# Kernel optimization log

Hardware: AMD Instinct MI355X
Metric: run time of the kernel (lower is better)

Reference implementation:

```python
import jax, jax.numpy as jnp
import numpy as np

C_IN = 256
C_INTER = C_IN // 2  # max(1, C//2)
B, D, H, W = 2, 16, 64, 64


def setup_inputs() -> dict:
    key = jax.random.key(0)
    ks = jax.random.split(key, 9)
    s = 1.0 / np.sqrt(C_IN)
    si = 1.0 / np.sqrt(C_INTER)
    return {
        "x": jax.random.normal(ks[0], (B, C_IN, D, H, W), dtype=jnp.float32),
        # 1x1x1 conv weights reduce to [out, in] matrices
        "g_w": jax.random.normal(ks[1], (C_INTER, C_IN), dtype=jnp.float32) * s,
        "g_b": jax.random.normal(ks[2], (C_INTER,), dtype=jnp.float32) * s,
        "theta_w": jax.random.normal(ks[3], (C_INTER, C_IN), dtype=jnp.float32) * s,
        "theta_b": jax.random.normal(ks[4], (C_INTER,), dtype=jnp.float32) * s,
        "phi_w": jax.random.normal(ks[5], (C_INTER, C_IN), dtype=jnp.float32) * s,
        "phi_b": jax.random.normal(ks[6], (C_INTER,), dtype=jnp.float32) * s,
        # note: torch code inits W to zero; random here so gradients/outputs are non-trivial
        "W_w": jax.random.normal(ks[7], (C_IN, C_INTER), dtype=jnp.float32) * si,
        "W_b": jax.random.normal(ks[8], (C_IN,), dtype=jnp.float32) * si,
    }


def reference(x, g_w, g_b, theta_w, theta_b, phi_w, phi_b, W_w, W_b):
    b, c, d, h, w = x.shape
    n = d * h * w
    xf = x.reshape(b, c, n)  # [B, C, N]
    # 1x1x1 convs == per-position linear projections
    g = jnp.einsum('oc,bcn->bon', g_w, xf) + g_b[None, :, None]        # [B, Ci, N]
    th = jnp.einsum('oc,bcn->bon', theta_w, xf) + theta_b[None, :, None]
    ph = jnp.einsum('oc,bcn->bon', phi_w, xf) + phi_b[None, :, None]
    # f = theta^T @ phi (N x N), y = (f / N) @ g^T. Since the normalizer is a
    # constant, reassociate: kv = phi @ g^T is [Ci, Ci], avoiding the NxN matrix.
    kv = jnp.einsum('bin,bjn->bij', ph, g)                              # [B, Ci, Ci]
    y = jnp.einsum('bin,bij->bjn', th, kv) / n                          # [B, Ci, N]
    y = jnp.einsum('oc,bcn->bon', W_w, y) + W_b[None, :, None]          # [B, C, N]
    return x + y.reshape(b, c, d, h, w)
```

## Files before the change

### kernel.cpp

```cpp
#include <hip/hip_runtime.h>

#define NB 2
#define CC 256
#define CI 128
#define NN 65536
#define LDA 72
#define LDX 264

typedef __bf16 bf16x8 __attribute__((ext_vector_type(8)));
typedef float f32x4 __attribute__((ext_vector_type(4)));

__device__ __forceinline__ unsigned short f2bf(float f) {
  unsigned u = __float_as_uint(f);
  u += 0x7fffu + ((u >> 16) & 1u);
  return (unsigned short)(u >> 16);
}

__global__ __launch_bounds__(512) void nl3d_syrk2(const float* __restrict__ x,
                                                  float* __restrict__ S,
                                                  float* __restrict__ partials,
                                                  float* __restrict__ svec,
                                                  int kchunk, int use_partial) {
  __shared__ unsigned short lds[256 * LDA];
  const int tid = threadIdx.x;
  const int lane = tid & 63;
  const int wv = tid >> 6;
  const int wm = wv & 3, wn = wv >> 2;
  const int b = blockIdx.y;
  const int kc0 = blockIdx.x * kchunk;

  const float* xb = x + (size_t)b * CC * NN;
  f32x4 acc[4][8];
  const f32x4 zero4 = {0.f, 0.f, 0.f, 0.f};
#pragma unroll
  for (int i = 0; i < 4; ++i)
#pragma unroll
    for (int j = 0; j < 8; ++j) acc[i][j] = zero4;

  float rsum[8];
#pragma unroll
  for (int i = 0; i < 8; ++i) rsum[i] = 0.f;

  const int r0 = tid >> 4;
  const int c4 = tid & 15;

  const int stages = kchunk >> 6;
  for (int s = 0; s < stages; ++s) {
    const int kc = kc0 + s * 64;
    float4 f[8];
#pragma unroll
    for (int i = 0; i < 8; ++i) {
      int row = r0 + 32 * i;
      f[i] = *(const float4*)(xb + (size_t)row * NN + kc + c4 * 4);
    }
    __syncthreads();
#pragma unroll
    for (int i = 0; i < 8; ++i) {
      int row = r0 + 32 * i;
      ushort4 h;
      h.x = f2bf(f[i].x); h.y = f2bf(f[i].y); h.z = f2bf(f[i].z); h.w = f2bf(f[i].w);
      *(ushort4*)&lds[row * LDA + c4 * 4] = h;
      rsum[i] += f[i].x + f[i].y + f[i].z + f[i].w;
    }
    __syncthreads();

    const int m = lane & 15;
    const int kg = (lane >> 4) * 8;
#pragma unroll
    for (int kk = 0; kk < 2; ++kk) {
      bf16x8 afr[4], bfr[8];
#pragma unroll
      for (int mt = 0; mt < 4; ++mt)
        afr[mt] = *(const bf16x8*)&lds[(wm * 64 + mt * 16 + m) * LDA + kk * 32 + kg];
#pragma unroll
      for (int nt = 0; nt < 8; ++nt)
        bfr[nt] = *(const bf16x8*)&lds[(wn * 128 + nt * 16 + m) * LDA + kk * 32 + kg];
#pragma unroll
      for (int mt = 0; mt < 4; ++mt)
#pragma unroll
        for (int nt = 0; nt < 8; ++nt)
          acc[mt][nt] = __builtin_amdgcn_mfma_f32_16x16x32_bf16(afr[mt], bfr[nt], acc[mt][nt], 0, 0, 0);
    }
  }

  const int col = lane & 15;
  const int rq = (lane >> 4) * 4;
  if (use_partial) {
    float* dst = partials + ((size_t)(b * gridDim.x + blockIdx.x)) * (CC * CC);
#pragma unroll
    for (int mt = 0; mt < 4; ++mt)
#pragma unroll
      for (int nt = 0; nt < 8; ++nt)
#pragma unroll
        for (int r = 0; r < 4; ++r) {
          int gi = wm * 64 + mt * 16 + rq + r;
          int gj = wn * 128 + nt * 16 + col;
          dst[gi * CC + gj] = acc[mt][nt][r];
        }
  } else {
    float* Sb = S + (size_t)b * CC * CC;
#pragma unroll
    for (int mt = 0; mt < 4; ++mt)
#pragma unroll
      for (int nt = 0; nt < 8; ++nt)
#pragma unroll
        for (int r = 0; r < 4; ++r) {
          int gi = wm * 64 + mt * 16 + rq + r;
          int gj = wn * 128 + nt * 16 + col;
          atomicAdd(&Sb[gi * CC + gj], acc[mt][nt][r]);
        }
  }

  __syncthreads();
  float* ldsRS = (float*)lds;
  if (tid < 256) ldsRS[tid] = 0.f;
  __syncthreads();
#pragma unroll
  for (int i = 0; i < 8; ++i) atomicAdd(&ldsRS[r0 + 32 * i], rsum[i]);
  __syncthreads();
  if (tid < 256) atomicAdd(&svec[b * CC + tid], ldsRS[tid]);
}

__global__ __launch_bounds__(256) void nl3d_reduce(const float* __restrict__ partials,
                                                   float* __restrict__ S, int splits) {
  const int e = blockIdx.x * 256 + threadIdx.x;
  const int b = e >> 14;
  const int off = e & 16383;
  const float4* p = (const float4*)partials;
  float4 a0 = {0, 0, 0, 0}, a1 = {0, 0, 0, 0};
  const size_t base = (size_t)b * splits * 16384 + off;
  for (int s = 0; s < splits; s += 2) {
    float4 v0 = p[base + (size_t)s * 16384];
    float4 v1 = p[base + (size_t)(s + 1) * 16384];
    a0.x += v0.x; a0.y += v0.y; a0.z += v0.z; a0.w += v0.w;
    a1.x += v1.x; a1.y += v1.y; a1.z += v1.z; a1.w += v1.w;
  }
  float4 r;
  r.x = a0.x + a1.x; r.y = a0.y + a1.y; r.z = a0.z + a1.z; r.w = a0.w + a1.w;
  ((float4*)S)[e] = r;
}

__global__ void nl3d_b0(const float* __restrict__ g_w, float* __restrict__ gwT) {
  int t = blockIdx.x * 256 + threadIdx.x;
  int j = t >> 8, d = t & 255;
  gwT[d * CI + j] = g_w[t];
}

__global__ void nl3d_b1(const float* __restrict__ phi_w, const float* __restrict__ S,
                        float* __restrict__ P) {
  int b = blockIdx.x >> 7, i = blockIdx.x & 127, d = threadIdx.x;
  const float* Sb = S + (size_t)b * CC * CC;
  const float* ph = phi_w + i * CC;
  float a0 = 0.f, a1 = 0.f, a2 = 0.f, a3 = 0.f;
  for (int c = 0; c < CC; c += 4) {
    a0 += ph[c + 0] * Sb[(c + 0) * CC + d];
    a1 += ph[c + 1] * Sb[(c + 1) * CC + d];
    a2 += ph[c + 2] * Sb[(c + 2) * CC + d];
    a3 += ph[c + 3] * Sb[(c + 3) * CC + d];
  }
  P[((size_t)b * CI + i) * CC + d] = (a0 + a1) + (a2 + a3);
}

__global__ void nl3d_b2(const float* __restrict__ P, const float* __restrict__ gwT,
                        const float* __restrict__ svec, const float* __restrict__ phi_w,
                        const float* __restrict__ phi_b, const float* __restrict__ g_b,
                        float* __restrict__ kv) {
  int b = blockIdx.x >> 7, i = blockIdx.x & 127, j = threadIdx.x;
  const float* Pr = P + ((size_t)b * CI + i) * CC;
  const float* sv = svec + b * CC;
  const float* ph = phi_w + i * CC;
  float u0 = 0.f, u1 = 0.f;
  for (int c = 0; c < CC; c += 2) {
    u0 += ph[c] * sv[c];
    u1 += ph[c + 1] * sv[c + 1];
  }
  float a0 = 0.f, a1 = 0.f, v0 = 0.f, v1 = 0.f;
  for (int d = 0; d < CC; d += 2) {
    float gT0 = gwT[d * CI + j], gT1 = gwT[(d + 1) * CI + j];
    a0 += Pr[d] * gT0; a1 += Pr[d + 1] * gT1;
    v0 += sv[d] * gT0; v1 += sv[d + 1] * gT1;
  }
  kv[((size_t)b * CI + i) * CI + j] =
      (a0 + a1) + (u0 + u1) * g_b[j] + phi_b[i] * ((v0 + v1) + (float)NN * g_b[j]);
}

__global__ void nl3d_b3(const float* __restrict__ kv, const float* __restrict__ theta_w,
                        const float* __restrict__ theta_b, float* __restrict__ T2,
                        float* __restrict__ tb2) {
  int b = blockIdx.x >> 7, j = blockIdx.x & 127, c = threadIdx.x;
  const float* kvb = kv + (size_t)b * CI * CI;
  float a0 = 0.f, a1 = 0.f;
  for (int i = 0; i < CI; i += 2) {
    a0 += kvb[i * CI + j] * theta_w[i * CC + c];
    a1 += kvb[(i + 1) * CI + j] * theta_w[(i + 1) * CC + c];
  }
  T2[((size_t)b * CI + j) * CC + c] = a0 + a1;
  if (c == 0) {
    float t = 0.f;
    for (int i = 0; i < CI; ++i) t += kvb[i * CI + j] * theta_b[i];
    tb2[b * CI + j] = t;
  }
}

__global__ void nl3d_b4(const float* __restrict__ T2, const float* __restrict__ tb2,
                        const float* __restrict__ W_w, const float* __restrict__ W_b,
                        unsigned short* __restrict__ Mbf, float* __restrict__ cvec) {
  int b = blockIdx.x >> 8, o = blockIdx.x & 255, c = threadIdx.x;
  const float inv = 1.0f / (float)NN;
  const float* Wr = W_w + o * CI;
  float a0 = 0.f, a1 = 0.f;
  for (int j = 0; j < CI; j += 2) {
    a0 += Wr[j] * T2[((size_t)b * CI + j) * CC + c];
    a1 += Wr[j + 1] * T2[((size_t)b * CI + j + 1) * CC + c];
  }
  Mbf[((size_t)b * CC + o) * CC + c] = f2bf((a0 + a1) * inv);
  if (c == 0) {
    float t = 0.f;
    for (int j = 0; j < CI; ++j) t += Wr[j] * tb2[b * CI + j];
    cvec[b * CC + o] = t * inv + W_b[o];
  }
}

__global__ __launch_bounds__(256) void nl3d_out(const float* __restrict__ x,
                                                const unsigned short* __restrict__ Mbf,
                                                const float* __restrict__ cvec,
                                                float* __restrict__ out) {
  __shared__ unsigned short xT[64 * LDX];
  const int tid = threadIdx.x;
  const int lane = tid & 63;
  const int wv = tid >> 6;
  const int b = blockIdx.y;
  const int n0 = blockIdx.x * 64;

  const float* xb = x + (size_t)b * CC * NN;
  float* ob = out + (size_t)b * CC * NN;

  {
    const int c4 = tid & 15;
#pragma unroll
    for (int i = 0; i < 8; ++i) {
      int p = i * 16 + (tid >> 4);
      float4 f0 = *(const float4*)(xb + (size_t)(2 * p) * NN + n0 + c4 * 4);
      float4 f1 = *(const float4*)(xb + (size_t)(2 * p + 1) * NN + n0 + c4 * 4);
      float a0[4] = {f0.x, f0.y, f0.z, f0.w};
      float a1[4] = {f1.x, f1.y, f1.z, f1.w};
      int ps = p ^ ((c4 & 7) << 2);
#pragma unroll
      for (int j = 0; j < 4; ++j) {
        unsigned pack = (unsigned)f2bf(a0[j]) | ((unsigned)f2bf(a1[j]) << 16);
        *(unsigned*)&xT[(c4 * 4 + j) * LDX + 2 * ps] = pack;
      }
    }
  }
  __syncthreads();

  f32x4 acc[4][4];
  const f32x4 zero4 = {0.f, 0.f, 0.f, 0.f};
#pragma unroll
  for (int i = 0; i < 4; ++i)
#pragma unroll
    for (int j = 0; j < 4; ++j) acc[i][j] = zero4;

  const int m = lane & 15;
  const int kg = (lane >> 4) * 8;
  const unsigned short* Mb = Mbf + (size_t)b * CC * CC;
#pragma unroll
  for (int kc = 0; kc < 8; ++kc) {
    bf16x8 afr[4], bfr[4];
#pragma unroll
    for (int mt = 0; mt < 4; ++mt)
      afr[mt] = *(const bf16x8*)(Mb + (size_t)(wv * 64 + mt * 16 + m) * CC + kc * 32 + kg);
#pragma unroll
    for (int nt = 0; nt < 4; ++nt) {
      int rr = nt * 16 + m;
      int d0 = (kc * 16 + (kg >> 1)) ^ (((rr >> 2) & 7) << 2);
      bfr[nt] = *(const bf16x8*)&xT[rr * LDX + 2 * d0];
    }
#pragma unroll
    for (int mt = 0; mt < 4; ++mt)
#pragma unroll
      for (int nt = 0; nt < 4; ++nt)
        acc[mt][nt] = __builtin_amdgcn_mfma_f32_16x16x32_bf16(afr[mt], bfr[nt], acc[mt][nt], 0, 0, 0);
  }

  const int col = lane & 15;
  const int rquad = (lane >> 4) * 4;
#pragma unroll
  for (int mt = 0; mt < 4; ++mt)
#pragma unroll
    for (int r = 0; r < 4; ++r) {
      int o = wv * 64 + mt * 16 + rquad + r;
      float cv = cvec[b * CC + o];
      const float* xrow = xb + (size_t)o * NN + n0;
      float* orow = ob + (size_t)o * NN + n0;
#pragma unroll
      for (int nt = 0; nt < 4; ++nt) {
        int n = nt * 16 + col;
        orow[n] = xrow[n] + acc[mt][nt][r] + cv;
      }
    }
}

extern "C" void kernel_launch(void* const* d_in, const int* in_sizes, int n_in,
                              void* d_out, int out_size, void* d_ws, size_t ws_size,
                              hipStream_t stream) {
  const float* x       = (const float*)d_in[0];
  const float* g_w     = (const float*)d_in[1];
  const float* g_b     = (const float*)d_in[2];
  const float* theta_w = (const float*)d_in[3];
  const float* theta_b = (const float*)d_in[4];
  const float* phi_w   = (const float*)d_in[5];
  const float* phi_b   = (const float*)d_in[6];
  const float* W_w     = (const float*)d_in[7];
  const float* W_b     = (const float*)d_in[8];
  float* out = (float*)d_out;

  char* ws = (char*)d_ws;
  float* S    = (float*)(ws);
  float* svec = (float*)(ws + 524288);
  float* P    = (float*)(ws + 526336);
  float* gwT  = (float*)(ws + 788480);
  float* kv   = (float*)(ws + 919552);
  float* T2   = (float*)(ws + 1050624);
  float* tb2  = (float*)(ws + 1312768);
  unsigned short* Mbf = (unsigned short*)(ws + 1313792);
  float* cvec = (float*)(ws + 1575936);
  float* partials = (float*)(ws + 2097152);

  int splits = 0;
  for (int c = 128; c >= 8; c >>= 1) {
    if (2097152 + (size_t)NB * c * CC * CC * 4 <= ws_size) { splits = c; break; }
  }

  if (splits > 0) {
    hipMemsetAsync(svec, 0, 2048, stream);
    nl3d_syrk2<<<dim3(splits, NB), 512, 0, stream>>>(x, S, partials, svec,
                                                     NN / splits, 1);
    nl3d_reduce<<<128, 256, 0, stream>>>(partials, S, splits);
  } else {
    hipMemsetAsync(ws, 0, 526336, stream);
    nl3d_syrk2<<<dim3(64, NB), 512, 0, stream>>>(x, S, (float*)ws, svec,
                                                 NN / 64, 0);
  }
  nl3d_b0<<<128, 256, 0, stream>>>(g_w, gwT);
  nl3d_b1<<<NB * CI, 256, 0, stream>>>(phi_w, S, P);
  nl3d_b2<<<NB * CI, 128, 0, stream>>>(P, gwT, svec, phi_w, phi_b, g_b, kv);
  nl3d_b3<<<NB * CI, 256, 0, stream>>>(kv, theta_w, theta_b, T2, tb2);
  nl3d_b4<<<NB * CC, 256, 0, stream>>>(T2, tb2, W_w, W_b, Mbf, cvec);
  nl3d_out<<<dim3(NN / 64, NB), 256, 0, stream>>>(x, Mbf, cvec, out);
}
```

Measured before the change: 394.4 us.

## Fuse small chain kernels with grid barriers, fold residual into M, pipeline loads

Merges the reduce and five small matrix-chain kernels into one persistent 256-block kernel that uses atomic-counter grid barriers, which cuts launch overhead. The identity is added into M, so the output kernel no longer re-reads x for the residual. The output kernel now handles four tiles per block with double-buffered register prefetch, and the syrk kernel gets a two-stage register prefetch. The grid barrier assumes all 256 blocks are co-resident. The residual is now computed in bf16, which lowers its precision.

```diff
diff --git a/kernel.cpp b/kernel.cpp
--- a/kernel.cpp
+++ b/kernel.cpp
@@ -43,17 +43,16 @@
 
   const int r0 = tid >> 4;
   const int c4 = tid & 15;
-
-  const int stages = kchunk >> 6;
-  for (int s = 0; s < stages; ++s) {
-    const int kc = kc0 + s * 64;
-    float4 f[8];
-#pragma unroll
-    for (int i = 0; i < 8; ++i) {
-      int row = r0 + 32 * i;
-      f[i] = *(const float4*)(xb + (size_t)row * NN + kc + c4 * 4);
-    }
-    __syncthreads();
+  const int m = lane & 15;
+  const int kg = (lane >> 4) * 8;
+
+  float4 fX0[8], fX1[8];
+  auto loadf = [&](float4* f, int kc) {
+#pragma unroll
+    for (int i = 0; i < 8; ++i)
+      f[i] = *(const float4*)(xb + (size_t)(r0 + 32 * i) * NN + kc + c4 * 4);
+  };
+  auto storef = [&](const float4* f) {
 #pragma unroll
     for (int i = 0; i < 8; ++i) {
       int row = r0 + 32 * i;
@@ -62,10 +61,8 @@
       *(ushort4*)&lds[row * LDA + c4 * 4] = h;
       rsum[i] += f[i].x + f[i].y + f[i].z + f[i].w;
     }
-    __syncthreads();
-
-    const int m = lane & 15;
-    const int kg = (lane >> 4) * 8;
+  };
+  auto mfma_blk = [&]() {
 #pragma unroll
     for (int kk = 0; kk < 2; ++kk) {
       bf16x8 afr[4], bfr[8];
@@ -81,6 +78,21 @@
         for (int nt = 0; nt < 8; ++nt)
           acc[mt][nt] = __builtin_amdgcn_mfma_f32_16x16x32_bf16(afr[mt], bfr[nt], acc[mt][nt], 0, 0, 0);
     }
+  };
+
+  const int stages = kchunk >> 6;
+  loadf(fX0, kc0);
+  for (int s = 0; s < stages; s += 2) {
+    __syncthreads();
+    storef(fX0);
+    if (s + 1 < stages) loadf(fX1, kc0 + (s + 1) * 64);
+    __syncthreads();
+    mfma_blk();
+    __syncthreads();
+    storef(fX1);
+    if (s + 2 < stages) loadf(fX0, kc0 + (s + 2) * 64);
+    __syncthreads();
+    mfma_blk();
   }
 
   const int col = lane & 15;
@@ -121,184 +133,257 @@
   if (tid < 256) atomicAdd(&svec[b * CC + tid], ldsRS[tid]);
 }
 
-__global__ __launch_bounds__(256) void nl3d_reduce(const float* __restrict__ partials,
-                                                   float* __restrict__ S, int splits) {
-  const int e = blockIdx.x * 256 + threadIdx.x;
-  const int b = e >> 14;
-  const int off = e & 16383;
-  const float4* p = (const float4*)partials;
-  float4 a0 = {0, 0, 0, 0}, a1 = {0, 0, 0, 0};
-  const size_t base = (size_t)b * splits * 16384 + off;
-  for (int s = 0; s < splits; s += 2) {
-    float4 v0 = p[base + (size_t)s * 16384];
-    float4 v1 = p[base + (size_t)(s + 1) * 16384];
-    a0.x += v0.x; a0.y += v0.y; a0.z += v0.z; a0.w += v0.w;
-    a1.x += v1.x; a1.y += v1.y; a1.z += v1.z; a1.w += v1.w;
-  }
-  float4 r;
-  r.x = a0.x + a1.x; r.y = a0.y + a1.y; r.z = a0.z + a1.z; r.w = a0.w + a1.w;
-  ((float4*)S)[e] = r;
-}
-
-__global__ void nl3d_b0(const float* __restrict__ g_w, float* __restrict__ gwT) {
-  int t = blockIdx.x * 256 + threadIdx.x;
-  int j = t >> 8, d = t & 255;
-  gwT[d * CI + j] = g_w[t];
-}
-
-__global__ void nl3d_b1(const float* __restrict__ phi_w, const float* __restrict__ S,
-                        float* __restrict__ P) {
-  int b = blockIdx.x >> 7, i = blockIdx.x & 127, d = threadIdx.x;
-  const float* Sb = S + (size_t)b * CC * CC;
-  const float* ph = phi_w + i * CC;
-  float a0 = 0.f, a1 = 0.f, a2 = 0.f, a3 = 0.f;
-  for (int c = 0; c < CC; c += 4) {
-    a0 += ph[c + 0] * Sb[(c + 0) * CC + d];
-    a1 += ph[c + 1] * Sb[(c + 1) * CC + d];
-    a2 += ph[c + 2] * Sb[(c + 2) * CC + d];
-    a3 += ph[c + 3] * Sb[(c + 3) * CC + d];
-  }
-  P[((size_t)b * CI + i) * CC + d] = (a0 + a1) + (a2 + a3);
-}
-
-__global__ void nl3d_b2(const float* __restrict__ P, const float* __restrict__ gwT,
-                        const float* __restrict__ svec, const float* __restrict__ phi_w,
-                        const float* __restrict__ phi_b, const float* __restrict__ g_b,
-                        float* __restrict__ kv) {
-  int b = blockIdx.x >> 7, i = blockIdx.x & 127, j = threadIdx.x;
-  const float* Pr = P + ((size_t)b * CI + i) * CC;
-  const float* sv = svec + b * CC;
-  const float* ph = phi_w + i * CC;
-  float u0 = 0.f, u1 = 0.f;
-  for (int c = 0; c < CC; c += 2) {
-    u0 += ph[c] * sv[c];
-    u1 += ph[c + 1] * sv[c + 1];
-  }
-  float a0 = 0.f, a1 = 0.f, v0 = 0.f, v1 = 0.f;
-  for (int d = 0; d < CC; d += 2) {
-    float gT0 = gwT[d * CI + j], gT1 = gwT[(d + 1) * CI + j];
-    a0 += Pr[d] * gT0; a1 += Pr[d + 1] * gT1;
-    v0 += sv[d] * gT0; v1 += sv[d + 1] * gT1;
-  }
-  kv[((size_t)b * CI + i) * CI + j] =
-      (a0 + a1) + (u0 + u1) * g_b[j] + phi_b[i] * ((v0 + v1) + (float)NN * g_b[j]);
-}
-
-__global__ void nl3d_b3(const float* __restrict__ kv, const float* __restrict__ theta_w,
-                        const float* __restrict__ theta_b, float* __restrict__ T2,
-                        float* __restrict__ tb2) {
-  int b = blockIdx.x >> 7, j = blockIdx.x & 127, c = threadIdx.x;
-  const float* kvb = kv + (size_t)b * CI * CI;
-  float a0 = 0.f, a1 = 0.f;
-  for (int i = 0; i < CI; i += 2) {
-    a0 += kvb[i * CI + j] * theta_w[i * CC + c];
-    a1 += kvb[(i + 1) * CI + j] * theta_w[(i + 1) * CC + c];
-  }
-  T2[((size_t)b * CI + j) * CC + c] = a0 + a1;
-  if (c == 0) {
-    float t = 0.f;
-    for (int i = 0; i < CI; ++i) t += kvb[i * CI + j] * theta_b[i];
-    tb2[b * CI + j] = t;
-  }
-}
-
-__global__ void nl3d_b4(const float* __restrict__ T2, const float* __restrict__ tb2,
-                        const float* __restrict__ W_w, const float* __restrict__ W_b,
-                        unsigned short* __restrict__ Mbf, float* __restrict__ cvec) {
-  int b = blockIdx.x >> 8, o = blockIdx.x & 255, c = threadIdx.x;
-  const float inv = 1.0f / (float)NN;
-  const float* Wr = W_w + o * CI;
-  float a0 = 0.f, a1 = 0.f;
-  for (int j = 0; j < CI; j += 2) {
-    a0 += Wr[j] * T2[((size_t)b * CI + j) * CC + c];
-    a1 += Wr[j + 1] * T2[((size_t)b * CI + j + 1) * CC + c];
-  }
-  Mbf[((size_t)b * CC + o) * CC + c] = f2bf((a0 + a1) * inv);
-  if (c == 0) {
-    float t = 0.f;
-    for (int j = 0; j < CI; ++j) t += Wr[j] * tb2[b * CI + j];
-    cvec[b * CC + o] = t * inv + W_b[o];
-  }
-}
-
-__global__ __launch_bounds__(256) void nl3d_out(const float* __restrict__ x,
-                                                const unsigned short* __restrict__ Mbf,
-                                                const float* __restrict__ cvec,
-                                                float* __restrict__ out) {
-  __shared__ unsigned short xT[64 * LDX];
+#define CHAIN_BLOCKS 256
+__device__ __forceinline__ void grid_barrier(unsigned* cnt, int phase) {
+  __syncthreads();
+  if (threadIdx.x == 0) {
+    __threadfence();
+    unsigned arrived = atomicAdd(&cnt[phase], 1u) + 1u;
+    if (arrived < (unsigned)CHAIN_BLOCKS) {
+      while (atomicAdd(&cnt[phase], 0u) < (unsigned)CHAIN_BLOCKS)
+        __builtin_amdgcn_s_sleep(1);
+    }
+    __threadfence();
+  }
+  __syncthreads();
+}
+
+__global__ __launch_bounds__(256) void nl3d_chain(
+    const float* __restrict__ partials, float* __restrict__ S,
+    const float* __restrict__ svec,
+    const float* __restrict__ g_w, float* __restrict__ gwT,
+    const float* __restrict__ phi_w, const float* __restrict__ phi_b,
+    const float* __restrict__ g_b,
+    const float* __restrict__ theta_w, const float* __restrict__ theta_b,
+    const float* __restrict__ W_w, const float* __restrict__ W_b,
+    float* __restrict__ P, float* __restrict__ kv, float* __restrict__ T2,
+    float* __restrict__ tb2, unsigned short* __restrict__ Mbf,
+    float* __restrict__ cvec, unsigned* __restrict__ cnt, int splits) {
+  const int tid = threadIdx.x;
+  const int bi = blockIdx.x;
+  const int gtid = bi * 256 + tid;
+  __shared__ float red[256];
+
+  if (splits > 0 && gtid < 32768) {
+    const int b = gtid >> 14, off = gtid & 16383;
+    const float4* p = (const float4*)partials;
+    const size_t base = (size_t)b * splits * 16384 + off;
+    float4 a0 = {0,0,0,0}, a1 = {0,0,0,0}, a2 = {0,0,0,0}, a3 = {0,0,0,0};
+    for (int s = 0; s < splits; s += 4) {
+      float4 v0 = p[base + (size_t)(s + 0) * 16384];
+      float4 v1 = p[base + (size_t)(s + 1) * 16384];
+      float4 v2 = p[base + (size_t)(s + 2) * 16384];
+      float4 v3 = p[base + (size_t)(s + 3) * 16384];
+      a0.x += v0.x; a0.y += v0.y; a0.z += v0.z; a0.w += v0.w;
+      a1.x += v1.x; a1.y += v1.y; a1.z += v1.z; a1.w += v1.w;
+      a2.x += v2.x; a2.y += v2.y; a2.z += v2.z; a2.w += v2.w;
+      a3.x += v3.x; a3.y += v3.y; a3.z += v3.z; a3.w += v3.w;
+    }
+    float4 r;
+    r.x = (a0.x + a1.x) + (a2.x + a3.x);
+    r.y = (a0.y + a1.y) + (a2.y + a3.y);
+    r.z = (a0.z + a1.z) + (a2.z + a3.z);
+    r.w = (a0.w + a1.w) + (a2.w + a3.w);
+    ((float4*)S)[gtid] = r;
+  }
+  if (gtid >= 32768) {
+    int t = gtid - 32768;
+    gwT[(t & 255) * CI + (t >> 8)] = g_w[t];
+  }
+  grid_barrier(cnt, 0);
+
+  {
+    const int b = bi >> 7, i = bi & 127, d = tid;
+    const float* Sb = S + (size_t)b * CC * CC;
+    const float* ph = phi_w + i * CC;
+    float a0 = 0, a1 = 0, a2 = 0, a3 = 0, a4 = 0, a5 = 0, a6 = 0, a7 = 0;
+    for (int c = 0; c < CC; c += 8) {
+      a0 += ph[c + 0] * Sb[(c + 0) * CC + d];
+      a1 += ph[c + 1] * Sb[(c + 1) * CC + d];
+      a2 += ph[c + 2] * Sb[(c + 2) * CC + d];
+      a3 += ph[c + 3] * Sb[(c + 3) * CC + d];
+      a4 += ph[c + 4] * Sb[(c + 4) * CC + d];
+      a5 += ph[c + 5] * Sb[(c + 5) * CC + d];
+      a6 += ph[c + 6] * Sb[(c + 6) * CC + d];
+      a7 += ph[c + 7] * Sb[(c + 7) * CC + d];
+    }
+    P[((size_t)b * CI + i) * CC + d] = ((a0 + a1) + (a2 + a3)) + ((a4 + a5) + (a6 + a7));
+  }
+  grid_barrier(cnt, 1);
+
+  {
+    const int b = bi >> 7, i = bi & 127;
+    if (tid < 128) {
+      const int j = tid;
+      const float* Pr = P + ((size_t)b * CI + i) * CC;
+      const float* sv = svec + b * CC;
+      const float* ph = phi_w + i * CC;
+      float u0 = 0, u1 = 0;
+      for (int c = 0; c < CC; c += 2) { u0 += ph[c] * sv[c]; u1 += ph[c + 1] * sv[c + 1]; }
+      float a0 = 0, a1 = 0, a2 = 0, a3 = 0, v0 = 0, v1 = 0, v2 = 0, v3 = 0;
+      for (int d = 0; d < CC; d += 4) {
+        float g0 = gwT[(d + 0) * CI + j], g1 = gwT[(d + 1) * CI + j];
+        float g2 = gwT[(d + 2) * CI + j], g3 = gwT[(d + 3) * CI + j];
+        a0 += Pr[d + 0] * g0; a1 += Pr[d + 1] * g1; a2 += Pr[d + 2] * g2; a3 += Pr[d + 3] * g3;
+        v0 += sv[d + 0] * g0; v1 += sv[d + 1] * g1; v2 += sv[d + 2] * g2; v3 += sv[d + 3] * g3;
+      }
+      kv[((size_t)b * CI + i) * CI + j] =
+          ((a0 + a1) + (a2 + a3)) + (u0 + u1) * g_b[j] +
+          phi_b[i] * (((v0 + v1) + (v2 + v3)) + (float)NN * g_b[j]);
+    }
+  }
+  grid_barrier(cnt, 2);
+
+  {
+    const int b = bi >> 7, j = bi & 127, c = tid;
+    const float* kvb = kv + (size_t)b * CI * CI;
+    float a0 = 0, a1 = 0, a2 = 0, a3 = 0;
+    for (int i = 0; i < CI; i += 4) {
+      a0 += kvb[(i + 0) * CI + j] * theta_w[(i + 0) * CC + c];
+      a1 += kvb[(i + 1) * CI + j] * theta_w[(i + 1) * CC + c];
+      a2 += kvb[(i + 2) * CI + j] * theta_w[(i + 2) * CC + c];
+      a3 += kvb[(i + 3) * CI + j] * theta_w[(i + 3) * CC + c];
+    }
+    T2[((size_t)b * CI + j) * CC + c] = (a0 + a1) + (a2 + a3);
+    red[tid] = (tid < CI) ? kvb[tid * CI + j] * theta_b[tid] : 0.f;
+    __syncthreads();
+    for (int s = 64; s > 0; s >>= 1) {
+      if (tid < s) red[tid] += red[tid + s];
+      __syncthreads();
+    }
+    if (tid == 0) tb2[b * CI + j] = red[0];
+    __syncthreads();
+  }
+  grid_barrier(cnt, 3);
+
+  {
+    const float inv = 1.0f / (float)NN;
+#pragma unroll
+    for (int oo = 0; oo < 2; ++oo) {
+      const int idx = bi * 2 + oo;
+      const int b = idx >> 8, o = idx & 255, c = tid;
+      const float* Wr = W_w + o * CI;
+      float a0 = 0, a1 = 0, a2 = 0, a3 = 0;
+      for (int j = 0; j < CI; j += 4) {
+        a0 += Wr[j + 0] * T2[((size_t)b * CI + j + 0) * CC + c];
+        a1 += Wr[j + 1] * T2[((size_t)b * CI + j + 1) * CC + c];
+        a2 += Wr[j + 2] * T2[((size_t)b * CI + j + 2) * CC + c];
+        a3 += Wr[j + 3] * T2[((size_t)b * CI + j + 3) * CC + c];
+      }
+      float mval = ((a0 + a1) + (a2 + a3)) * inv + (o == c ? 1.0f : 0.0f);
+      Mbf[((size_t)b * CC + o) * CC + c] = f2bf(mval);
+      red[tid] = (tid < CI) ? Wr[tid] * tb2[b * CI + tid] : 0.f;
+      __syncthreads();
+      for (int s = 64; s > 0; s >>= 1) {
+        if (tid < s) red[tid] += red[tid + s];
+        __syncthreads();
+      }
+      if (tid == 0) cvec[b * CC + o] = red[0] * inv + W_b[o];
+      __syncthreads();
+    }
+  }
+}
+
+__global__ __launch_bounds__(256, 2) void nl3d_out(const float* __restrict__ x,
+                                                   const unsigned short* __restrict__ Mbf,
+                                                   const float* __restrict__ cvec,
+                                                   float* __restrict__ out) {
+  __shared__ unsigned short xT[2][64 * LDX];
   const int tid = threadIdx.x;
   const int lane = tid & 63;
   const int wv = tid >> 6;
   const int b = blockIdx.y;
-  const int n0 = blockIdx.x * 64;
+  const int n_base = blockIdx.x * 256;
 
   const float* xb = x + (size_t)b * CC * NN;
   float* ob = out + (size_t)b * CC * NN;
-
-  {
-    const int c4 = tid & 15;
-#pragma unroll
-    for (int i = 0; i < 8; ++i) {
-      int p = i * 16 + (tid >> 4);
-      float4 f0 = *(const float4*)(xb + (size_t)(2 * p) * NN + n0 + c4 * 4);
-      float4 f1 = *(const float4*)(xb + (size_t)(2 * p + 1) * NN + n0 + c4 * 4);
-      float a0[4] = {f0.x, f0.y, f0.z, f0.w};
-      float a1[4] = {f1.x, f1.y, f1.z, f1.w};
-      int ps = p ^ ((c4 & 7) << 2);
-#pragma unroll
-      for (int j = 0; j < 4; ++j) {
-        unsigned pack = (unsigned)f2bf(a0[j]) | ((unsigned)f2bf(a1[j]) << 16);
-        *(unsigned*)&xT[(c4 * 4 + j) * LDX + 2 * ps] = pack;
-      }
-    }
-  }
-  __syncthreads();
-
-  f32x4 acc[4][4];
-  const f32x4 zero4 = {0.f, 0.f, 0.f, 0.f};
-#pragma unroll
-  for (int i = 0; i < 4; ++i)
-#pragma unroll
-    for (int j = 0; j < 4; ++j) acc[i][j] = zero4;
-
+  const unsigned short* Mb = Mbf + (size_t)b * CC * CC;
+
+  const int c4 = tid & 15;
+  const int pr = tid >> 4;
   const int m = lane & 15;
   const int kg = (lane >> 4) * 8;
-  const unsigned short* Mb = Mbf + (size_t)b * CC * CC;
-#pragma unroll
-  for (int kc = 0; kc < 8; ++kc) {
-    bf16x8 afr[4], bfr[4];
-#pragma unroll
-    for (int mt = 0; mt < 4; ++mt)
-      afr[mt] = *(const bf16x8*)(Mb + (size_t)(wv * 64 + mt * 16 + m) * CC + kc * 32 + kg);
-#pragma unroll
-    for (int nt = 0; nt < 4; ++nt) {
-      int rr = nt * 16 + m;
-      int d0 = (kc * 16 + (kg >> 1)) ^ (((rr >> 2) & 7) << 2);
-      bfr[nt] = *(const bf16x8*)&xT[rr * LDX + 2 * d0];
-    }
-#pragma unroll
-    for (int mt = 0; mt < 4; ++mt)
-#pragma unroll
-      for (int nt = 0; nt < 4; ++nt)
-        acc[mt][nt] = __builtin_amdgcn_mfma_f32_16x16x32_bf16(afr[mt], bfr[nt], acc[mt][nt], 0, 0, 0);
-  }
-
   const int col = lane & 15;
   const int rquad = (lane >> 4) * 4;
+
+  float cvf[4][4];
 #pragma unroll
   for (int mt = 0; mt < 4; ++mt)
 #pragma unroll
-    for (int r = 0; r < 4; ++r) {
-      int o = wv * 64 + mt * 16 + rquad + r;
-      float cv = cvec[b * CC + o];
-      const float* xrow = xb + (size_t)o * NN + n0;
-      float* orow = ob + (size_t)o * NN + n0;
+    for (int r = 0; r < 4; ++r)
+      cvf[mt][r] = cvec[b * CC + wv * 64 + mt * 16 + rquad + r];
+
+  float4 fa[2][8], fb[2][8];
+  auto load_tile = [&](int t, int buf) {
+    const int n0 = n_base + t * 64;
+#pragma unroll
+    for (int i = 0; i < 8; ++i) {
+      const int p = i * 16 + pr;
+      fa[buf][i] = *(const float4*)(xb + (size_t)(2 * p) * NN + n0 + c4 * 4);
+      fb[buf][i] = *(const float4*)(xb + (size_t)(2 * p + 1) * NN + n0 + c4 * 4);
+    }
+  };
+
+  load_tile(0, 0);
+  const f32x4 zero4 = {0.f, 0.f, 0.f, 0.f};
+
+#pragma unroll
+  for (int t = 0; t < 4; ++t) {
+    const int buf = t & 1;
+    __syncthreads();
+#pragma unroll
+    for (int i = 0; i < 8; ++i) {
+      const int p = i * 16 + pr;
+      const int ps = p ^ ((c4 & 7) << 2);
+      float A0[4] = {fa[buf][i].x, fa[buf][i].y, fa[buf][i].z, fa[buf][i].w};
+      float A1[4] = {fb[buf][i].x, fb[buf][i].y, fb[buf][i].z, fb[buf][i].w};
+#pragma unroll
+      for (int j = 0; j < 4; ++j) {
+        unsigned pack = (unsigned)f2bf(A0[j]) | ((unsigned)f2bf(A1[j]) << 16);
+        *(unsigned*)&xT[buf][(c4 * 4 + j) * LDX + 2 * ps] = pack;
+      }
+    }
+    if (t < 3) load_tile(t + 1, buf ^ 1);
+    __syncthreads();
+
+    f32x4 acc[4][4];
+#pragma unroll
+    for (int i = 0; i < 4; ++i)
+#pragma unroll
+      for (int j = 0; j < 4; ++j) acc[i][j] = zero4;
+
+#pragma unroll
+    for (int kc = 0; kc < 8; ++kc) {
+      bf16x8 afr[4], bfr[4];
+#pragma unroll
+      for (int mt = 0; mt < 4; ++mt)
+        afr[mt] = *(const bf16x8*)(Mb + (size_t)(wv * 64 + mt * 16 + m) * CC + kc * 32 + kg);
 #pragma unroll
       for (int nt = 0; nt < 4; ++nt) {
-        int n = nt * 16 + col;
-        orow[n] = xrow[n] + acc[mt][nt][r] + cv;
-      }
-    }
+        const int rr = nt * 16 + m;
+        const int d0 = (kc * 16 + (kg >> 1)) ^ (((rr >> 2) & 7) << 2);
+        bfr[nt] = *(const bf16x8*)&xT[buf][rr * LDX + 2 * d0];
+      }
+#pragma unroll
+      for (int mt = 0; mt < 4; ++mt)
+#pragma unroll
+        for (int nt = 0; nt < 4; ++nt)
+          acc[mt][nt] = __builtin_amdgcn_mfma_f32_16x16x32_bf16(afr[mt], bfr[nt], acc[mt][nt], 0, 0, 0);
+    }
+
+    const int n0 = n_base + t * 64;
+#pragma unroll
+    for (int mt = 0; mt < 4; ++mt)
+#pragma unroll
+      for (int r = 0; r < 4; ++r) {
+        const int o = wv * 64 + mt * 16 + rquad + r;
+        float* orow = ob + (size_t)o * NN + n0;
+        const float cv = cvf[mt][r];
+#pragma unroll
+        for (int nt = 0; nt < 4; ++nt)
+          orow[nt * 16 + col] = acc[mt][nt][r] + cv;
+      }
+  }
 }
 
 extern "C" void kernel_launch(void* const* d_in, const int* in_sizes, int n_in,
@@ -325,6 +410,7 @@
   float* tb2  = (float*)(ws + 1312768);
   unsigned short* Mbf = (unsigned short*)(ws + 1313792);
   float* cvec = (float*)(ws + 1575936);
+  unsigned* cnt = (unsigned*)(ws + 1577984);
   float* partials = (float*)(ws + 2097152);
 
   int splits = 0;
@@ -333,19 +419,16 @@
   }
 
   if (splits > 0) {
-    hipMemsetAsync(svec, 0, 2048, stream);
+    hipMemsetAsync(ws + 524288, 0, 1578240 - 524288, stream);
     nl3d_syrk2<<<dim3(splits, NB), 512, 0, stream>>>(x, S, partials, svec,
                                                      NN / splits, 1);
-    nl3d_reduce<<<128, 256, 0, stream>>>(partials, S, splits);
   } else {
-    hipMemsetAsync(ws, 0, 526336, stream);
+    hipMemsetAsync(ws, 0, 1578240, stream);
     nl3d_syrk2<<<dim3(64, NB), 512, 0, stream>>>(x, S, (float*)ws, svec,
                                                  NN / 64, 0);
   }
-  nl3d_b0<<<128, 256, 0, stream>>>(g_w, gwT);
-  nl3d_b1<<<NB * CI, 256, 0, stream>>>(phi_w, S, P);
-  nl3d_b2<<<NB * CI, 128, 0, stream>>>(P, gwT, svec, phi_w, phi_b, g_b, kv);
-  nl3d_b3<<<NB * CI, 256, 0, stream>>>(kv, theta_w, theta_b, T2, tb2);
-  nl3d_b4<<<NB * CC, 256, 0, stream>>>(T2, tb2, W_w, W_b, Mbf, cvec);
-  nl3d_out<<<dim3(NN / 64, NB), 256, 0, stream>>>(x, Mbf, cvec, out);
-}
+  nl3d_chain<<<CHAIN_BLOCKS, 256, 0, stream>>>(
+      partials, S, svec, g_w, gwT, phi_w, phi_b, g_b, theta_w, theta_b,
+      W_w, W_b, P, kv, T2, tb2, Mbf, cvec, cnt, splits);
+  nl3d_out<<<dim3(NN / 256, NB), 256, 0, stream>>>(x, Mbf, cvec, out);
+}
```

After: 524.9 us. +33.1%, slower.
